# Kernel tuning notes

Measured on AMD Instinct MI355X. Metric: run time of the kernel, lower is better.

Reference implementation:

```python
import jax, jax.numpy as jnp
import numpy as np

N = 4096      # nodes
HID = 512     # hidden_size
HEADS = 8
DH = HID // HEADS
EPS = 1e-5    # BatchNorm eps


def setup_inputs() -> dict:
    key = jax.random.key(0)
    ks = jax.random.split(key, 16)
    h = jax.random.normal(ks[0], (N, HID), jnp.float32)
    # sparse adjacency (~degree 32) with self-loops so every row has a neighbor
    A = (jax.random.uniform(ks[1], (N, N)) < 0.008).astype(jnp.float32)
    A = jnp.maximum(A, jnp.eye(N, dtype=jnp.float32))
    w = lambda k, shp: jax.random.normal(k, shp, jnp.float32) * 0.02
    return {
        "A": A, "h": h,
        "Wq": w(ks[2], (HID, HID)), "bq": jnp.zeros((HID,), jnp.float32),
        "Wk": w(ks[3], (HID, HID)), "bk": jnp.zeros((HID,), jnp.float32),
        "Wv": w(ks[4], (HID, HID)), "bv": jnp.zeros((HID,), jnp.float32),
        "Wo": w(ks[5], (HID, HID)), "bo": jnp.zeros((HID,), jnp.float32),
        "bn1_g": jnp.ones((HID,), jnp.float32), "bn1_b": jnp.zeros((HID,), jnp.float32),
        "bn2_g": jnp.ones((HID,), jnp.float32), "bn2_b": jnp.zeros((HID,), jnp.float32),
        "W1": w(ks[6], (HID, 2 * HID)), "b1": jnp.zeros((2 * HID,), jnp.float32),
        "W2": w(ks[7], (2 * HID, HID)), "b2": jnp.zeros((HID,), jnp.float32),
    }


def _batchnorm(x, g, b):
    # BatchNorm1d training mode: stats over the node (batch) axis
    m = jnp.mean(x, axis=0)
    v = jnp.var(x, axis=0)
    return g * (x - m) * jax.lax.rsqrt(v + EPS) + b


def _layer(A, h, Wq, bq, Wk, bk, Wv, bv, Wo, bo,
           bn1_g, bn1_b, bn2_g, bn2_b, W1, b1, W2, b2):
    n = h.shape[0]
    q = (h @ Wq + bq).reshape(n, HEADS, DH)
    k = (h @ Wk + bk).reshape(n, HEADS, DH)
    v = (h @ Wv + bv).reshape(n, HEADS, DH)
    # scores [heads, n, m], masked by adjacency
    scores = jnp.einsum('nhd,mhd->hnm', q, k) / np.float32(np.sqrt(DH))
    scores = jnp.where(A[None, :, :] > 0, scores, jnp.float32(-1e9))
    attn = jax.nn.softmax(scores, axis=-1)
    o = jnp.einsum('hnm,mhd->nhd', attn, v).reshape(n, HID)
    h1 = o @ Wo + bo
    h = _batchnorm(h + h1, bn1_g, bn1_b)
    h2 = jax.nn.relu(h @ W1 + b1) @ W2 + b2
    return _batchnorm(h + h2, bn2_g, bn2_b)


def reference(A, h, Wq, bq, Wk, bk, Wv, bv, Wo, bo,
              bn1_g, bn1_b, bn2_g, bn2_b, W1, b1, W2, b2):
    return _layer(A, h, Wq, bq, Wk, bk, Wv, bv, Wo, bo,
                  bn1_g, bn1_b, bn2_g, bn2_b, W1, b1, W2, b2)
```

## Files before the change

kernel.cpp:

```cpp
#include <hip/hip_runtime.h>

#define N_NODES 4096
#define HID 512
#define HEADS 8
#define DH 64
#define EPS 1e-5f
#define MAXD 128

typedef __attribute__((ext_vector_type(8))) short bf16x8;
typedef __attribute__((ext_vector_type(4))) float f32x4;

__device__ __forceinline__ unsigned short f2bf(float f) {
    unsigned int u = __float_as_uint(f);
    unsigned int r = (u + 0x7FFFu + ((u >> 16) & 1u)) >> 16;
    return (unsigned short)r;
}
__device__ __forceinline__ float blo(unsigned int u) {
    return __uint_as_float(u << 16);
}
__device__ __forceinline__ float bhi(unsigned int u) {
    return __uint_as_float(u & 0xffff0000u);
}

__device__ __forceinline__ void gld_lds16(const void* g, void* l) {
    __builtin_amdgcn_global_load_lds(
        (const __attribute__((address_space(1))) unsigned int*)g,
        (__attribute__((address_space(3))) unsigned int*)l, 16, 0, 0);
}

template<int TM, int EPI>
__global__ __launch_bounds__(256) void gemm_bf16(
    const unsigned short* __restrict__ Xb, const unsigned short* __restrict__ Wt,
    const float* __restrict__ bias, const float* __restrict__ res,
    const unsigned short* __restrict__ resb,
    float* __restrict__ outf, unsigned short* __restrict__ outb,
    float* __restrict__ sum, float* __restrict__ sumsq,
    int K, int Nc)
{
    constexpr int WM = TM / 64;
    __shared__ __align__(16) unsigned short As[TM * 64];
    __shared__ __align__(16) unsigned short Bs[64 * 64];

    const int tid = threadIdx.x;
    const int lane = tid & 63;
    const int wv = tid >> 6;
    const int m0 = blockIdx.y * TM, n0 = blockIdx.x * 64;
    const int lc = lane & 15, lq = lane >> 4;
    const int rowbase = wv * (WM * 16);

    const int srow = tid >> 3;
    const int schunk = (tid & 7) ^ (srow & 7);
    unsigned short* ldsA = As + tid * 8;
    unsigned short* ldsB = Bs + tid * 8;
    const int rs0 = lq ^ (lc & 7);
    const int rs1 = (4 + lq) ^ (lc & 7);

    f32x4 acc[WM][4] = {};

    for (int k0 = 0; k0 < K; k0 += 64) {
        const unsigned short* gA = Xb + (size_t)(m0 + srow) * K + k0 + schunk * 8;
        const unsigned short* gB = Wt + (size_t)(n0 + srow) * K + k0 + schunk * 8;
        #pragma unroll
        for (int p = 0; p < TM / 32; ++p)
            gld_lds16(gA + (size_t)(p * 32) * K, ldsA + p * 2048);
        #pragma unroll
        for (int p = 0; p < 2; ++p)
            gld_lds16(gB + (size_t)(p * 32) * K, ldsB + p * 2048);
        __syncthreads();

        #pragma unroll
        for (int hh = 0; hh < 2; ++hh) {
            const int rs = hh ? rs1 : rs0;
            bf16x8 af[WM], bfr[4];
            #pragma unroll
            for (int i = 0; i < WM; ++i)
                af[i] = *(const bf16x8*)&As[(rowbase + i * 16 + lc) * 64 + rs * 8];
            #pragma unroll
            for (int j = 0; j < 4; ++j)
                bfr[j] = *(const bf16x8*)&Bs[(j * 16 + lc) * 64 + rs * 8];
            #pragma unroll
            for (int i = 0; i < WM; ++i)
                #pragma unroll
                for (int j = 0; j < 4; ++j)
                    acc[i][j] = __builtin_amdgcn_mfma_f32_16x16x32_bf16(af[i], bfr[j], acc[i][j], 0, 0, 0);
        }
        __syncthreads();
    }

    float cs[4] = {}, css[4] = {};
    #pragma unroll
    for (int i = 0; i < WM; ++i) {
        #pragma unroll
        for (int j = 0; j < 4; ++j) {
            const int gr0 = m0 + rowbase + i * 16 + lq * 4;
            const int gc = n0 + j * 16 + lc;
            const float bi = bias[gc];
            #pragma unroll
            for (int r = 0; r < 4; ++r) {
                float val = acc[i][j][r] + bi;
                size_t off = (size_t)(gr0 + r) * Nc + gc;
                if (EPI == 0)      outb[off] = f2bf(val);
                else if (EPI == 1) outb[off] = f2bf(fmaxf(val, 0.f));
                else {
                    if (EPI == 2) val += res[off];
                    else          val += blo((unsigned int)resb[off]);
                    outf[off] = val;
                    cs[j] += val; css[j] += val * val;
                }
            }
        }
    }
    if (EPI >= 2) {
        #pragma unroll
        for (int j = 0; j < 4; ++j) {
            float s = cs[j], ss = css[j];
            s += __shfl_xor(s, 16); s += __shfl_xor(s, 32);
            ss += __shfl_xor(ss, 16); ss += __shfl_xor(ss, 32);
            if (lq == 0) {
                const int gc = n0 + j * 16 + lc;
                atomicAdd(&sum[gc], s);
                atomicAdd(&sumsq[gc], ss);
            }
        }
    }
}

__global__ __launch_bounds__(256) void prep_all(
    const float* __restrict__ Wq, const float* __restrict__ Wk,
    const float* __restrict__ Wv, const float* __restrict__ Wo,
    const float* __restrict__ W1, const float* __restrict__ W2,
    const float* __restrict__ h,
    const float* __restrict__ bq, const float* __restrict__ bk,
    const float* __restrict__ bv,
    unsigned short* __restrict__ wqkvT, unsigned short* __restrict__ woT,
    unsigned short* __restrict__ w1T, unsigned short* __restrict__ w2T,
    unsigned int* __restrict__ hb, float* __restrict__ bqkv,
    float* __restrict__ st)
{
    const int z = blockIdx.z;
    if (z < 6) {
        const float* in; unsigned short* out; int R, C;
        switch (z) {
            case 0: in = Wq; out = wqkvT;          R = 512;  C = 512;  break;
            case 1: in = Wk; out = wqkvT + 262144; R = 512;  C = 512;  break;
            case 2: in = Wv; out = wqkvT + 524288; R = 512;  C = 512;  break;
            case 3: in = Wo; out = woT;            R = 512;  C = 512;  break;
            case 4: in = W1; out = w1T;            R = 512;  C = 1024; break;
            default: in = W2; out = w2T;           R = 1024; C = 512;  break;
        }
        const int bc = blockIdx.x * 32, br = blockIdx.y * 32;
        if (bc >= C || br >= R) return;
        __shared__ float tile[32][33];
        const int tx = threadIdx.x & 31, ty = threadIdx.x >> 5;
        #pragma unroll
        for (int r = ty; r < 32; r += 8)
            tile[r][tx] = in[(size_t)(br + r) * C + bc + tx];
        __syncthreads();
        #pragma unroll
        for (int r = ty; r < 32; r += 8)
            out[(size_t)(bc + r) * R + br + tx] = f2bf(tile[tx][r]);
    } else if (z == 6) {
        const int blk = blockIdx.y * 32 + blockIdx.x;
        const int i = blk * 512 + threadIdx.x * 2;
        const float4* in4 = (const float4*)h;
        #pragma unroll
        for (int u = 0; u < 2; ++u) {
            float4 f = in4[i + u];
            hb[(i + u) * 2]     = (unsigned int)f2bf(f.x) | ((unsigned int)f2bf(f.y) << 16);
            hb[(i + u) * 2 + 1] = (unsigned int)f2bf(f.z) | ((unsigned int)f2bf(f.w) << 16);
        }
    } else {
        const int blk = blockIdx.y * 32 + blockIdx.x;
        const int i = blk * 256 + threadIdx.x;
        if (i < 1536) bqkv[i] = i < 512 ? bq[i] : (i < 1024 ? bk[i - 512] : bv[i - 1024]);
        if (i < 2048) st[i] = 0.0f;
    }
}

__global__ __launch_bounds__(256) void sparse_attn5(
    const float* __restrict__ A, const unsigned short* __restrict__ qkv,
    unsigned short* __restrict__ o)
{
    const int n = blockIdx.x;
    const int tid = threadIdx.x;
    const int wv = tid >> 6, lane = tid & 63;

    __shared__ int s_idx[MAXD];
    __shared__ float s_p[8][MAXD];
    __shared__ int s_cnt[4];

    const float4* r4 = (const float4*)(A + (size_t)n * N_NODES);
    float4 av[4];
    #pragma unroll
    for (int t = 0; t < 4; ++t)
        av[t] = r4[wv * 256 + t * 64 + lane];

    const unsigned long long lt = (1ull << lane) - 1ull;
    int cnt = 0;
    #pragma unroll
    for (int t = 0; t < 4; ++t) {
        #pragma unroll
        for (int b = 0; b < 4; ++b) {
            float vb = (b == 0) ? av[t].x : (b == 1) ? av[t].y : (b == 2) ? av[t].z : av[t].w;
            cnt += __popcll(__ballot(vb > 0.0f));
        }
    }
    if (lane == 0) s_cnt[wv] = cnt;
    __syncthreads();
    int base = 0, total = 0;
    #pragma unroll
    for (int w = 0; w < 4; ++w) {
        if (w < wv) base += s_cnt[w];
        total += s_cnt[w];
    }
    const int d = total < MAXD ? total : MAXD;
    #pragma unroll
    for (int t = 0; t < 4; ++t) {
        #pragma unroll
        for (int b = 0; b < 4; ++b) {
            float vb = (b == 0) ? av[t].x : (b == 1) ? av[t].y : (b == 2) ? av[t].z : av[t].w;
            unsigned long long m = __ballot(vb > 0.0f);
            if (vb > 0.0f) {
                int p = base + __popcll(m & lt);
                if (p < MAXD) s_idx[p] = wv * 1024 + t * 256 + lane * 4 + b;
            }
            base += __popcll(m);
        }
    }
    __syncthreads();

    const int jl = lane >> 3;
    const int dgs = lane & 7;
    const int jl2 = lane >> 4;
    const int dga = lane & 15;
    const int h0 = wv, h1 = wv + 4;

    const unsigned short* qp = qkv + (size_t)n * 1536 + dgs * 8;
    uint4 qa = *(const uint4*)(qp + h0 * 64);
    uint4 qb = *(const uint4*)(qp + h1 * 64);
    const float a0 = blo(qa.x), a1 = bhi(qa.x), a2 = blo(qa.y), a3 = bhi(qa.y);
    const float a4 = blo(qa.z), a5 = bhi(qa.z), a6 = blo(qa.w), a7 = bhi(qa.w);
    const float b0 = blo(qb.x), b1 = bhi(qb.x), b2 = blo(qb.y), b3 = bhi(qb.y);
    const float b4 = blo(qb.z), b5 = bhi(qb.z), b6 = blo(qb.w), b7 = bhi(qb.w);

    uint4 ka = {0, 0, 0, 0}, kb = {0, 0, 0, 0};
    if (jl < d) {
        const unsigned short* p = qkv + (size_t)s_idx[jl] * 1536 + 512 + dgs * 8;
        ka = *(const uint4*)(p + h0 * 64);
        kb = *(const uint4*)(p + h1 * 64);
    }
    for (int j0 = 0; j0 < d; j0 += 8) {
        const uint4 ca = ka, cb = kb;
        const int jn = j0 + 8 + jl;
        if (jn < d) {
            const unsigned short* p = qkv + (size_t)s_idx[jn] * 1536 + 512 + dgs * 8;
            ka = *(const uint4*)(p + h0 * 64);
            kb = *(const uint4*)(p + h1 * 64);
        }
        const int jc = j0 + jl;
        float s0 = 0.f, s1 = 0.f;
        if (jc < d) {
            s0 = a0 * blo(ca.x) + a1 * bhi(ca.x) + a2 * blo(ca.y) + a3 * bhi(ca.y)
               + a4 * blo(ca.z) + a5 * bhi(ca.z) + a6 * blo(ca.w) + a7 * bhi(ca.w);
            s1 = b0 * blo(cb.x) + b1 * bhi(cb.x) + b2 * blo(cb.y) + b3 * bhi(cb.y)
               + b4 * blo(cb.z) + b5 * bhi(cb.z) + b6 * blo(cb.w) + b7 * bhi(cb.w);
        }
        s0 += __shfl_xor(s0, 1); s1 += __shfl_xor(s1, 1);
        s0 += __shfl_xor(s0, 2); s1 += __shfl_xor(s1, 2);
        s0 += __shfl_xor(s0, 4); s1 += __shfl_xor(s1, 4);
        if (dgs == 0 && jc < d) {
            s_p[h0][jc] = s0 * 0.125f;
            s_p[h1][jc] = s1 * 0.125f;
        }
    }

    float inv0, inv1;
    #pragma unroll
    for (int hh = 0; hh < 2; ++hh) {
        float* sp = s_p[hh ? h1 : h0];
        float mx = -1e30f;
        for (int j = lane; j < d; j += 64) mx = fmaxf(mx, sp[j]);
        #pragma unroll
        for (int off = 32; off; off >>= 1) mx = fmaxf(mx, __shfl_xor(mx, off));
        float sum = 0.f;
        for (int j = lane; j < d; j += 64) {
            float e = __expf(sp[j] - mx);
            sp[j] = e;
            sum += e;
        }
        #pragma unroll
        for (int off = 32; off; off >>= 1) sum += __shfl_xor(sum, off);
        if (hh) inv1 = 1.0f / sum; else inv0 = 1.0f / sum;
    }

    float x0 = 0.f, x1 = 0.f, x2 = 0.f, x3 = 0.f;
    float y0 = 0.f, y1 = 0.f, y2 = 0.f, y3 = 0.f;
    uint2 va = {0, 0}, vb = {0, 0};
    if (jl2 < d) {
        const unsigned short* p = qkv + (size_t)s_idx[jl2] * 1536 + 1024 + dga * 4;
        va = *(const uint2*)(p + h0 * 64);
        vb = *(const uint2*)(p + h1 * 64);
    }
    for (int j0 = 0; j0 < d; j0 += 4) {
        const uint2 ca = va, cb = vb;
        const int jn = j0 + 4 + jl2;
        if (jn < d) {
            const unsigned short* p = qkv + (size_t)s_idx[jn] * 1536 + 1024 + dga * 4;
            va = *(const uint2*)(p + h0 * 64);
            vb = *(const uint2*)(p + h1 * 64);
        }
        const int jc = j0 + jl2;
        if (jc < d) {
            const float p0 = s_p[h0][jc], p1 = s_p[h1][jc];
            x0 += p0 * blo(ca.x); x1 += p0 * bhi(ca.x);
            x2 += p0 * blo(ca.y); x3 += p0 * bhi(ca.y);
            y0 += p1 * blo(cb.x); y1 += p1 * bhi(cb.x);
            y2 += p1 * blo(cb.y); y3 += p1 * bhi(cb.y);
        }
    }
    x0 += __shfl_xor(x0, 16); x0 += __shfl_xor(x0, 32);
    x1 += __shfl_xor(x1, 16); x1 += __shfl_xor(x1, 32);
    x2 += __shfl_xor(x2, 16); x2 += __shfl_xor(x2, 32);
    x3 += __shfl_xor(x3, 16); x3 += __shfl_xor(x3, 32);
    y0 += __shfl_xor(y0, 16); y0 += __shfl_xor(y0, 32);
    y1 += __shfl_xor(y1, 16); y1 += __shfl_xor(y1, 32);
    y2 += __shfl_xor(y2, 16); y2 += __shfl_xor(y2, 32);
    y3 += __shfl_xor(y3, 16); y3 += __shfl_xor(y3, 32);
    if (jl2 == 0) {
        uint2 w0, w1;
        w0.x = (unsigned int)f2bf(x0 * inv0) | ((unsigned int)f2bf(x1 * inv0) << 16);
        w0.y = (unsigned int)f2bf(x2 * inv0) | ((unsigned int)f2bf(x3 * inv0) << 16);
        w1.x = (unsigned int)f2bf(y0 * inv1) | ((unsigned int)f2bf(y1 * inv1) << 16);
        w1.y = (unsigned int)f2bf(y2 * inv1) | ((unsigned int)f2bf(y3 * inv1) << 16);
        *(uint2*)(o + (size_t)n * 512 + h0 * 64 + dga * 4) = w0;
        *(uint2*)(o + (size_t)n * 512 + h1 * 64 + dga * 4) = w1;
    }
}

__global__ __launch_bounds__(256) void bn_apply4(
    const float4* __restrict__ x, const float* __restrict__ sum,
    const float* __restrict__ sumsq, const float* __restrict__ g,
    const float* __restrict__ b, float4* __restrict__ yf,
    uint2* __restrict__ yb)
{
    const int i = blockIdx.x * 256 + threadIdx.x;
    const int c4 = i & 127;
    const float4 s4 = ((const float4*)sum)[c4];
    const float4 q4 = ((const float4*)sumsq)[c4];
    const float4 g4 = ((const float4*)g)[c4];
    const float4 b4 = ((const float4*)b)[c4];
    const float4 xv = x[i];
    const float kN = 1.0f / N_NODES;
    float4 r;
    { float m = s4.x * kN; r.x = g4.x * (xv.x - m) * rsqrtf(q4.x * kN - m * m + EPS) + b4.x; }
    { float m = s4.y * kN; r.y = g4.y * (xv.y - m) * rsqrtf(q4.y * kN - m * m + EPS) + b4.y; }
    { float m = s4.z * kN; r.z = g4.z * (xv.z - m) * rsqrtf(q4.z * kN - m * m + EPS) + b4.z; }
    { float m = s4.w * kN; r.w = g4.w * (xv.w - m) * rsqrtf(q4.w * kN - m * m + EPS) + b4.w; }
    if (yf) yf[i] = r;
    if (yb) {
        uint2 p;
        p.x = (unsigned int)f2bf(r.x) | ((unsigned int)f2bf(r.y) << 16);
        p.y = (unsigned int)f2bf(r.z) | ((unsigned int)f2bf(r.w) << 16);
        yb[i] = p;
    }
}


extern "C" void kernel_launch(void* const* d_in, const int* in_sizes, int n_in,
                              void* d_out, int out_size, void* d_ws, size_t ws_size,
                              hipStream_t stream)
{
    const float* A   = (const float*)d_in[0];
    const float* h   = (const float*)d_in[1];
    const float* Wq  = (const float*)d_in[2];
    const float* bq  = (const float*)d_in[3];
    const float* Wk  = (const float*)d_in[4];
    const float* bk  = (const float*)d_in[5];
    const float* Wv  = (const float*)d_in[6];
    const float* bv  = (const float*)d_in[7];
    const float* Wo  = (const float*)d_in[8];
    const float* bo  = (const float*)d_in[9];
    const float* g1  = (const float*)d_in[10];
    const float* b1g = (const float*)d_in[11];
    const float* g2  = (const float*)d_in[12];
    const float* b2g = (const float*)d_in[13];
    const float* W1  = (const float*)d_in[14];
    const float* b1  = (const float*)d_in[15];
    const float* W2  = (const float*)d_in[16];
    const float* b2  = (const float*)d_in[17];
    float* out = (float*)d_out;

    float* ws = (float*)d_ws;
    unsigned short* hb    = (unsigned short*)(ws);
    unsigned short* qkvb  = (unsigned short*)(ws + 1048576);
    unsigned short* o_bf  = (unsigned short*)(ws + 4194304);
    unsigned short* wqkvT = (unsigned short*)(ws + 5242880);
    unsigned short* woT   = (unsigned short*)(ws + 5636096);
    unsigned short* w1T   = (unsigned short*)(ws + 5767168);
    unsigned short* w2T   = (unsigned short*)(ws + 6029312);
    unsigned short* t_b   = (unsigned short*)(ws + 6291456);
    float* x1   = ws + 8388608;
    float* x2   = ws + 10485760;
    unsigned short* xb1_b = (unsigned short*)(ws + 12582912);
    float* bqkv = ws + 13631488;
    float* st   = ws + 13633024;

    prep_all<<<dim3(32, 32, 8), dim3(256), 0, stream>>>(
        Wq, Wk, Wv, Wo, W1, W2, h, bq, bk, bv,
        wqkvT, woT, w1T, w2T, (unsigned int*)hb, bqkv, st);

    gemm_bf16<128, 0><<<dim3(24, 32), dim3(256), 0, stream>>>(
        hb, wqkvT, bqkv, nullptr, nullptr, nullptr, qkvb, nullptr, nullptr, 512, 1536);

    sparse_attn5<<<dim3(N_NODES), dim3(256), 0, stream>>>(A, qkvb, o_bf);

    gemm_bf16<64, 2><<<dim3(8, 64), dim3(256), 0, stream>>>(
        o_bf, woT, bo, h, nullptr, x1, nullptr, st, st + 512, 512, 512);

    bn_apply4<<<dim3(2048), dim3(256), 0, stream>>>(
        (const float4*)x1, st, st + 512, g1, b1g, nullptr, (uint2*)xb1_b);

    gemm_bf16<128, 1><<<dim3(16, 32), dim3(256), 0, stream>>>(
        xb1_b, w1T, b1, nullptr, nullptr, nullptr, t_b, nullptr, nullptr, 512, 1024);

    gemm_bf16<64, 3><<<dim3(8, 64), dim3(256), 0, stream>>>(
        t_b, w2T, b2, nullptr, xb1_b, x2, nullptr, st + 1024, st + 1536, 1024, 512);

    bn_apply4<<<dim3(2048), dim3(256), 0, stream>>>(
        (const float4*)x2, st + 1024, st + 1536, g2, b2g, (float4*)out, nullptr);

    (void)in_sizes; (void)n_in; (void)out_size; (void)ws_size;
}
```

Measured before the change: 230.5 us.

## Overlap adjacency compaction with QKV GEMM via extra grid slice

Adjacency row scanning and neighbor-index compaction move out of the attention kernel into a second z-slice of the QKV GEMM launch. The 64 MB dense adjacency read then runs alongside the QKV matmul instead of serially inside attention. The attention kernel now only loads a compact index list and count per node. The cost is extra scratch traffic for the index arrays, which reuse the t_b workspace region. Overlap is also not guaranteed, because the scanning blocks may be scheduled after the GEMM blocks.

```diff
diff --git a/kernel.cpp b/kernel.cpp
--- a/kernel.cpp
+++ b/kernel.cpp
@@ -28,20 +28,71 @@
         (__attribute__((address_space(3))) unsigned int*)l, 16, 0, 0);
 }
 
-template<int TM, int EPI>
+template<int TM, int EPI, int ADJ>
 __global__ __launch_bounds__(256) void gemm_bf16(
     const unsigned short* __restrict__ Xb, const unsigned short* __restrict__ Wt,
     const float* __restrict__ bias, const float* __restrict__ res,
     const unsigned short* __restrict__ resb,
     float* __restrict__ outf, unsigned short* __restrict__ outb,
     float* __restrict__ sum, float* __restrict__ sumsq,
-    int K, int Nc)
+    int K, int Nc,
+    const float* __restrict__ Adj, int* __restrict__ adjIdx,
+    int* __restrict__ adjCnt)
 {
+    const int tid = threadIdx.x;
+
+    if (ADJ && blockIdx.z == 1) {
+        const int lane = tid & 63;
+        const int wv4 = tid >> 6;
+        __shared__ int s_cnt[4];
+        const unsigned long long lt = (1ull << lane) - 1ull;
+        const int nb = gridDim.x * gridDim.y;
+        for (int n = blockIdx.y * gridDim.x + blockIdx.x; n < N_NODES; n += nb) {
+            const float4* r4 = (const float4*)(Adj + (size_t)n * N_NODES);
+            float4 av[4];
+            #pragma unroll
+            for (int t = 0; t < 4; ++t)
+                av[t] = r4[wv4 * 256 + t * 64 + lane];
+            int cnt = 0;
+            #pragma unroll
+            for (int t = 0; t < 4; ++t) {
+                #pragma unroll
+                for (int b = 0; b < 4; ++b) {
+                    float vb = (b == 0) ? av[t].x : (b == 1) ? av[t].y : (b == 2) ? av[t].z : av[t].w;
+                    cnt += __popcll(__ballot(vb > 0.0f));
+                }
+            }
+            if (lane == 0) s_cnt[wv4] = cnt;
+            __syncthreads();
+            int base = 0, total = 0;
+            #pragma unroll
+            for (int w = 0; w < 4; ++w) {
+                if (w < wv4) base += s_cnt[w];
+                total += s_cnt[w];
+            }
+            #pragma unroll
+            for (int t = 0; t < 4; ++t) {
+                #pragma unroll
+                for (int b = 0; b < 4; ++b) {
+                    float vb = (b == 0) ? av[t].x : (b == 1) ? av[t].y : (b == 2) ? av[t].z : av[t].w;
+                    unsigned long long m = __ballot(vb > 0.0f);
+                    if (vb > 0.0f) {
+                        int p = base + __popcll(m & lt);
+                        if (p < MAXD) adjIdx[n * MAXD + p] = wv4 * 1024 + t * 256 + lane * 4 + b;
+                    }
+                    base += __popcll(m);
+                }
+            }
+            if (tid == 0) adjCnt[n] = total < MAXD ? total : MAXD;
+            __syncthreads();
+        }
+        return;
+    }
+
     constexpr int WM = TM / 64;
     __shared__ __align__(16) unsigned short As[TM * 64];
     __shared__ __align__(16) unsigned short Bs[64 * 64];
 
-    const int tid = threadIdx.x;
     const int lane = tid & 63;
     const int wv = tid >> 6;
     const int m0 = blockIdx.y * TM, n0 = blockIdx.x * 64;
@@ -177,9 +228,9 @@
     }
 }
 
-__global__ __launch_bounds__(256) void sparse_attn5(
-    const float* __restrict__ A, const unsigned short* __restrict__ qkv,
-    unsigned short* __restrict__ o)
+__global__ __launch_bounds__(256) void sparse_attn6(
+    const int* __restrict__ adjIdx, const int* __restrict__ adjCnt,
+    const unsigned short* __restrict__ qkv, unsigned short* __restrict__ o)
 {
     const int n = blockIdx.x;
     const int tid = threadIdx.x;
@@ -187,46 +238,9 @@
 
     __shared__ int s_idx[MAXD];
     __shared__ float s_p[8][MAXD];
-    __shared__ int s_cnt[4];
-
-    const float4* r4 = (const float4*)(A + (size_t)n * N_NODES);
-    float4 av[4];
-    #pragma unroll
-    for (int t = 0; t < 4; ++t)
-        av[t] = r4[wv * 256 + t * 64 + lane];
-
-    const unsigned long long lt = (1ull << lane) - 1ull;
-    int cnt = 0;
-    #pragma unroll
-    for (int t = 0; t < 4; ++t) {
-        #pragma unroll
-        for (int b = 0; b < 4; ++b) {
-            float vb = (b == 0) ? av[t].x : (b == 1) ? av[t].y : (b == 2) ? av[t].z : av[t].w;
-            cnt += __popcll(__ballot(vb > 0.0f));
-        }
-    }
-    if (lane == 0) s_cnt[wv] = cnt;
-    __syncthreads();
-    int base = 0, total = 0;
-    #pragma unroll
-    for (int w = 0; w < 4; ++w) {
-        if (w < wv) base += s_cnt[w];
-        total += s_cnt[w];
-    }
-    const int d = total < MAXD ? total : MAXD;
-    #pragma unroll
-    for (int t = 0; t < 4; ++t) {
-        #pragma unroll
-        for (int b = 0; b < 4; ++b) {
-            float vb = (b == 0) ? av[t].x : (b == 1) ? av[t].y : (b == 2) ? av[t].z : av[t].w;
-            unsigned long long m = __ballot(vb > 0.0f);
-            if (vb > 0.0f) {
-                int p = base + __popcll(m & lt);
-                if (p < MAXD) s_idx[p] = wv * 1024 + t * 256 + lane * 4 + b;
-            }
-            base += __popcll(m);
-        }
-    }
+
+    const int d = adjCnt[n];
+    if (tid < d) s_idx[tid] = adjIdx[n * MAXD + tid];
     __syncthreads();
 
     const int jl = lane >> 3;
@@ -404,27 +418,33 @@
     unsigned short* xb1_b = (unsigned short*)(ws + 12582912);
     float* bqkv = ws + 13631488;
     float* st   = ws + 13633024;
+    int* adjIdx = (int*)(ws + 6291456);
+    int* adjCnt = (int*)(ws + 6815744);
 
     prep_all<<<dim3(32, 32, 8), dim3(256), 0, stream>>>(
         Wq, Wk, Wv, Wo, W1, W2, h, bq, bk, bv,
         wqkvT, woT, w1T, w2T, (unsigned int*)hb, bqkv, st);
 
-    gemm_bf16<128, 0><<<dim3(24, 32), dim3(256), 0, stream>>>(
-        hb, wqkvT, bqkv, nullptr, nullptr, nullptr, qkvb, nullptr, nullptr, 512, 1536);
-
-    sparse_attn5<<<dim3(N_NODES), dim3(256), 0, stream>>>(A, qkvb, o_bf);
-
-    gemm_bf16<64, 2><<<dim3(8, 64), dim3(256), 0, stream>>>(
-        o_bf, woT, bo, h, nullptr, x1, nullptr, st, st + 512, 512, 512);
+    gemm_bf16<128, 0, 1><<<dim3(24, 32, 2), dim3(256), 0, stream>>>(
+        hb, wqkvT, bqkv, nullptr, nullptr, nullptr, qkvb, nullptr, nullptr,
+        512, 1536, A, adjIdx, adjCnt);
+
+    sparse_attn6<<<dim3(N_NODES), dim3(256), 0, stream>>>(adjIdx, adjCnt, qkvb, o_bf);
+
+    gemm_bf16<64, 2, 0><<<dim3(8, 64), dim3(256), 0, stream>>>(
+        o_bf, woT, bo, h, nullptr, x1, nullptr, st, st + 512,
+        512, 512, nullptr, nullptr, nullptr);
 
     bn_apply4<<<dim3(2048), dim3(256), 0, stream>>>(
         (const float4*)x1, st, st + 512, g1, b1g, nullptr, (uint2*)xb1_b);
 
-    gemm_bf16<128, 1><<<dim3(16, 32), dim3(256), 0, stream>>>(
-        xb1_b, w1T, b1, nullptr, nullptr, nullptr, t_b, nullptr, nullptr, 512, 1024);
-
-    gemm_bf16<64, 3><<<dim3(8, 64), dim3(256), 0, stream>>>(
-        t_b, w2T, b2, nullptr, xb1_b, x2, nullptr, st + 1024, st + 1536, 1024, 512);
+    gemm_bf16<128, 1, 0><<<dim3(16, 32), dim3(256), 0, stream>>>(
+        xb1_b, w1T, b1, nullptr, nullptr, nullptr, t_b, nullptr, nullptr,
+        512, 1024, nullptr, nullptr, nullptr);
+
+    gemm_bf16<64, 3, 0><<<dim3(8, 64), dim3(256), 0, stream>>>(
+        t_b, w2T, b2, nullptr, xb1_b, x2, nullptr, st + 1024, st + 1536,
+        1024, 512, nullptr, nullptr, nullptr);
 
     bn_apply4<<<dim3(2048), dim3(256), 0, stream>>>(
         (const float4*)x2, st + 1024, st + 1536, g2, b2g, (float4*)out, nullptr);
```

After: 233.3 us. Within noise of the previous version (+1.2%).
